# Optimization experiments

Measured on AMD Instinct MI355X. Metric: run time of the kernel, lower is better.

The kernel has to match this reference:

```python
import jax, jax.numpy as jnp
import numpy as np

KH, KW = 5, 5  # hardcoded in the module's build()


def setup_inputs() -> dict:
    key = jax.random.key(0)
    k1, k2 = jax.random.split(key)
    # inputs are cast to int32 inside call(); use integer-valued floats so the
    # cast is meaningful (pixel-like values in [0, 256)).
    inputs = jax.random.randint(k1, (4, 224, 224, 16), 0, 256).astype(jnp.float32)
    # learned kernel, shape (5, 5, C_in, filters); small signed integer values
    kernel = jax.random.randint(k2, (5, 5, 16, 32), -8, 8).astype(jnp.float32)
    return {"inputs": inputs, "kernel": kernel}


def reference(inputs, kernel):
    # Faithful int32 math: cast inputs and kernel to int32 as in call().
    x = inputs.astype(jnp.int32)            # [B, H, W, C]
    k = kernel.astype(jnp.int32)            # [KH, KW, C, F]
    B, H, W, C = x.shape
    F = k.shape[-1]
    Ho, Wo = H - KH + 1, W - KW + 1         # VALID 2D cross-correlation
    # Per-(channel, filter) conv with NO reduction over channels: fuse the
    # C_in*F separate MyConv2D launches into one vectorized 25-tap accumulation.
    out = jnp.zeros((B, Ho, Wo, C, F), dtype=jnp.int32)
    for i in range(KH):
        for j in range(KW):
            out = out + x[:, i:i + Ho, j:j + Wo, :, None] * k[i, j, :, :]
    # tf.stack(filters, axis=2) then tf.stack(channels, axis=2) produces
    # output layout [B, Ho, C, F, Wo].
    out = jnp.transpose(out, (0, 1, 3, 4, 2))
    return out.astype(jnp.float32)
```

## Files before the change

kernel.cpp:

```cpp
#include <hip/hip_runtime.h>

#define KH 5
#define KW 5
#define CIN 16
#define NF 32
#define H 224
#define W 224
#define HO 220
#define WO 220
#define RPB 4
#define XROWS (RPB + KH - 1)
#define WPAD 32

__global__ void transpose_weights(const float* __restrict__ Kw,
                                  float* __restrict__ Wt) {
    int idx = blockIdx.x * 256 + threadIdx.x;
    if (idx < KH * KW * CIN * NF) {
        const int tap = idx / (CIN * NF);
        const int rem = idx - tap * (CIN * NF);
        const int c   = rem >> 5;
        const int f   = rem & 31;
        Wt[((size_t)(c * NF) + f) * WPAD + tap] = Kw[idx];
    }
}

__global__ __launch_bounds__(256, 4) void conv2d_main(
    const float* __restrict__ X,
    const float* __restrict__ Wt,
    float* __restrict__ O)
{
    __shared__ float xs[XROWS * W];

    const int c   = blockIdx.x;
    const int ho0 = blockIdx.y * RPB;
    const int b   = blockIdx.z;
    const int t   = threadIdx.x;

    const float* xbase = X + ((size_t)(b * H + ho0) * W) * CIN + c;
    for (int idx = t; idx < XROWS * W; idx += 256)
        xs[idx] = xbase[(size_t)idx * CIN];
    __syncthreads();

    const int wave = t >> 6;
    const int lane = t & 63;
    const int wo0  = lane * 4;
    if (lane >= 55) return;

    float xw[KH][8];
#pragma unroll
    for (int i = 0; i < KH; ++i) {
        const float4 xa = *(const float4*)&xs[(wave + i) * W + wo0];
        const float4 xb = *(const float4*)&xs[(wave + i) * W + wo0 + 4];
        xw[i][0] = xa.x; xw[i][1] = xa.y; xw[i][2] = xa.z; xw[i][3] = xa.w;
        xw[i][4] = xb.x; xw[i][5] = xb.y; xw[i][6] = xb.z; xw[i][7] = xb.w;
    }

    const size_t obase =
        (((size_t)(b * HO + ho0 + wave) * CIN + c) * NF) * WO + wo0;
    const float* wc = Wt + (size_t)(c * NF) * WPAD;

#pragma unroll 2
    for (int f = 0; f < NF; ++f) {
        const float* wp = wc + (size_t)f * WPAD;
        float wk[KH * KW];
#pragma unroll
        for (int tap = 0; tap < KH * KW; ++tap)
            wk[tap] = wp[tap];

        float a0 = 0.0f, a1 = 0.0f, a2 = 0.0f, a3 = 0.0f;
#pragma unroll
        for (int i = 0; i < KH; ++i)
#pragma unroll
            for (int j = 0; j < KW; ++j) {
                const float w = wk[i * KW + j];
                a0 += xw[i][j + 0] * w;
                a1 += xw[i][j + 1] * w;
                a2 += xw[i][j + 2] * w;
                a3 += xw[i][j + 3] * w;
            }

        *(float4*)&O[obase + (size_t)f * WO] = make_float4(a0, a1, a2, a3);
    }
}

extern "C" void kernel_launch(void* const* d_in, const int* in_sizes, int n_in,
                              void* d_out, int out_size, void* d_ws, size_t ws_size,
                              hipStream_t stream) {
    const float* X  = (const float*)d_in[0];
    const float* Kw = (const float*)d_in[1];
    float* O        = (float*)d_out;
    float* Wt       = (float*)d_ws;

    transpose_weights<<<dim3(50), 256, 0, stream>>>(Kw, Wt);
    dim3 grid(CIN, HO / RPB, 4);
    conv2d_main<<<grid, 256, 0, stream>>>(X, Wt, O);
}
```

Baseline: 476.7 us.

## Split filters across waves, compute all rows per thread, swizzle blocks by XCD

Each wave now computes 8 filters for all 4 output rows instead of 32 filters for one row. Each thread keeps 8 input rows in registers and reuses each weight load across 4 rows. This cuts scalar weight loads per FMA. A 1D grid with an XCD-aware block remap is added, 32-bit index math replaces size_t, and the occupancy hint in launch bounds is dropped. Register pressure rises (64 input values plus 16 accumulators), which may reduce occupancy. The output-store pattern also changes.

```diff
diff --git a/kernel.cpp b/kernel.cpp
--- a/kernel.cpp
+++ b/kernel.cpp
@@ -11,6 +11,10 @@
 #define RPB 4
 #define XROWS (RPB + KH - 1)
 #define WPAD 32
+#define NTILE (HO / RPB)
+#define NBLK (CIN * NTILE * 4)
+#define NXCD 8
+#define CPX (NBLK / NXCD)
 
 __global__ void transpose_weights(const float* __restrict__ Kw,
                                   float* __restrict__ Wt) {
@@ -24,21 +28,25 @@
     }
 }
 
-__global__ __launch_bounds__(256, 4) void conv2d_main(
+__global__ __launch_bounds__(256) void conv2d_main(
     const float* __restrict__ X,
     const float* __restrict__ Wt,
     float* __restrict__ O)
 {
     __shared__ float xs[XROWS * W];
 
-    const int c   = blockIdx.x;
-    const int ho0 = blockIdx.y * RPB;
-    const int b   = blockIdx.z;
+    const int bid = blockIdx.x;
+    const int l   = (bid & 7) * CPX + (bid >> 3);
+    const int c   = l & 15;
+    const int rest = l >> 4;
+    const int hoT = rest % NTILE;
+    const int b   = rest / NTILE;
+    const int ho0 = hoT * RPB;
     const int t   = threadIdx.x;
 
-    const float* xbase = X + ((size_t)(b * H + ho0) * W) * CIN + c;
+    const uint32_t xoff = ((uint32_t)(b * H + ho0) * W) * CIN + c;
     for (int idx = t; idx < XROWS * W; idx += 256)
-        xs[idx] = xbase[(size_t)idx * CIN];
+        xs[idx] = X[xoff + (uint32_t)idx * CIN];
     __syncthreads();
 
     const int wave = t >> 6;
@@ -46,40 +54,55 @@
     const int wo0  = lane * 4;
     if (lane >= 55) return;
 
-    float xw[KH][8];
+    float xr[XROWS][8];
 #pragma unroll
-    for (int i = 0; i < KH; ++i) {
-        const float4 xa = *(const float4*)&xs[(wave + i) * W + wo0];
-        const float4 xb = *(const float4*)&xs[(wave + i) * W + wo0 + 4];
-        xw[i][0] = xa.x; xw[i][1] = xa.y; xw[i][2] = xa.z; xw[i][3] = xa.w;
-        xw[i][4] = xb.x; xw[i][5] = xb.y; xw[i][6] = xb.z; xw[i][7] = xb.w;
+    for (int r = 0; r < XROWS; ++r) {
+        const float4 xa = *(const float4*)&xs[r * W + wo0];
+        const float4 xb = *(const float4*)&xs[r * W + wo0 + 4];
+        xr[r][0] = xa.x; xr[r][1] = xa.y; xr[r][2] = xa.z; xr[r][3] = xa.w;
+        xr[r][4] = xb.x; xr[r][5] = xb.y; xr[r][6] = xb.z; xr[r][7] = xb.w;
     }
 
-    const size_t obase =
-        (((size_t)(b * HO + ho0 + wave) * CIN + c) * NF) * WO + wo0;
+    uint32_t obase[RPB];
+#pragma unroll
+    for (int r = 0; r < RPB; ++r)
+        obase[r] = (((uint32_t)(b * HO + ho0 + r) * CIN + c) * NF) * WO + wo0;
+
     const float* wc = Wt + (size_t)(c * NF) * WPAD;
 
-#pragma unroll 2
-    for (int f = 0; f < NF; ++f) {
+#pragma unroll 1
+    for (int fi = 0; fi < 8; ++fi) {
+        const int f = __builtin_amdgcn_readfirstlane(wave * 8 + fi);
         const float* wp = wc + (size_t)f * WPAD;
         float wk[KH * KW];
 #pragma unroll
         for (int tap = 0; tap < KH * KW; ++tap)
             wk[tap] = wp[tap];
 
-        float a0 = 0.0f, a1 = 0.0f, a2 = 0.0f, a3 = 0.0f;
+        float acc[RPB][4];
+#pragma unroll
+        for (int r = 0; r < RPB; ++r)
+#pragma unroll
+            for (int q = 0; q < 4; ++q) acc[r][q] = 0.0f;
+
 #pragma unroll
         for (int i = 0; i < KH; ++i)
 #pragma unroll
             for (int j = 0; j < KW; ++j) {
                 const float w = wk[i * KW + j];
-                a0 += xw[i][j + 0] * w;
-                a1 += xw[i][j + 1] * w;
-                a2 += xw[i][j + 2] * w;
-                a3 += xw[i][j + 3] * w;
+#pragma unroll
+                for (int r = 0; r < RPB; ++r) {
+                    acc[r][0] += xr[r + i][j + 0] * w;
+                    acc[r][1] += xr[r + i][j + 1] * w;
+                    acc[r][2] += xr[r + i][j + 2] * w;
+                    acc[r][3] += xr[r + i][j + 3] * w;
+                }
             }
 
-        *(float4*)&O[obase + (size_t)f * WO] = make_float4(a0, a1, a2, a3);
+#pragma unroll
+        for (int r = 0; r < RPB; ++r)
+            *(float4*)&O[obase[r] + (uint32_t)f * WO] =
+                make_float4(acc[r][0], acc[r][1], acc[r][2], acc[r][3]);
     }
 }
 
@@ -92,6 +115,5 @@
     float* Wt       = (float*)d_ws;
 
     transpose_weights<<<dim3(50), 256, 0, stream>>>(Kw, Wt);
-    dim3 grid(CIN, HO / RPB, 4);
-    conv2d_main<<<grid, 256, 0, stream>>>(X, Wt, O);
+    conv2d_main<<<dim3(NBLK), 256, 0, stream>>>(X, Wt, O);
 }
```

New measurement: 449.7 us. 5.7% less time.
